# Performance work log

Measured on AMD Instinct MI355X. Metric: run time of the kernel, lower is better.

Reference implementation:

```python
import jax, jax.numpy as jnp
import numpy as np

N_EMBD = 1024
HIDDEN = 4 * N_EMBD          # 4096
ADAPT = HIDDEN // 16         # 256
NUM_EXPERTS = 8
B, S = 4, 2048
LN_EPS = 1e-5


def setup_inputs() -> dict:
    key = jax.random.key(0)
    ks = jax.random.split(key, 8)
    x = jax.random.normal(ks[0], (B, S, N_EMBD), dtype=jnp.float32)
    # top-1 routing: one-hot expert weights (disjoint masks, standard MoE dispatch)
    route = jax.random.randint(ks[1], (B, S), 0, NUM_EXPERTS)
    expert_weights = jax.nn.one_hot(route, NUM_EXPERTS, dtype=jnp.float32)
    up_scale = 0.1 / N_EMBD ** 0.5
    adapt_scale0 = 0.1 / HIDDEN ** 0.5
    adapt_scale = 0.01 / ADAPT ** 0.5
    W_up = jax.random.normal(ks[2], (HIDDEN, N_EMBD), dtype=jnp.float32) * up_scale
    W_adapt = jax.random.normal(ks[3], (ADAPT, HIDDEN), dtype=jnp.float32) * adapt_scale0
    W_exp_adapters = jax.random.normal(ks[4], (NUM_EXPERTS, ADAPT, ADAPT), dtype=jnp.float32) * adapt_scale
    ln_gamma = jnp.ones((NUM_EXPERTS, ADAPT), dtype=jnp.float32)
    ln_beta = jnp.zeros((NUM_EXPERTS, ADAPT), dtype=jnp.float32)
    W_expert_proj = jax.random.normal(ks[5], (HIDDEN, ADAPT), dtype=jnp.float32) * adapt_scale
    W_out = jax.random.normal(ks[6], (N_EMBD, HIDDEN), dtype=jnp.float32) * adapt_scale
    return {"x": x, "expert_weights": expert_weights, "W_up": W_up,
            "W_adapt": W_adapt, "W_exp_adapters": W_exp_adapters,
            "ln_gamma": ln_gamma, "ln_beta": ln_beta,
            "W_expert_proj": W_expert_proj, "W_out": W_out}


def reference(x, expert_weights, W_up, W_adapt, W_exp_adapters, ln_gamma, ln_beta, W_expert_proj, W_out):
    b, s, d = x.shape
    T = b * s
    E = expert_weights.shape[-1]
    xt = x.reshape(T, d)

    # shared MLP path (silu(up_proj(x))) -> output_proj
    h = jax.nn.silu(xt @ W_up.T)                      # [T, HIDDEN]
    shared_out = (h @ W_out.T).reshape(b, s, d)       # [B, S, D]

    active = expert_weights.reshape(T, E) > 0         # [T, E]
    any_active = jnp.any(active, axis=-1)             # [T]
    last_idx = E - 1 - jnp.argmax(active[:, ::-1], axis=-1)  # [T]

    # pre_adapt (silu(up) recomputed == h) -> adapt_proj
    a = h @ W_adapt.T                                 # [T, ADAPT]
    # per-expert adapter linears, then select the winning expert per token
    a_all = jnp.einsum('td,eod->teo', a, W_exp_adapters)      # [T, E, ADAPT]
    a_sel = jnp.take_along_axis(a_all, last_idx[:, None, None], axis=1)[:, 0]  # [T, ADAPT]

    # per-expert LayerNorm params gathered per token
    g = ln_gamma[last_idx]                            # [T, ADAPT]
    be = ln_beta[last_idx]
    mu = jnp.mean(a_sel, axis=-1, keepdims=True)
    var = jnp.mean(jnp.square(a_sel - mu), axis=-1, keepdims=True)
    a_norm = (a_sel - mu) * jax.lax.rsqrt(var + LN_EPS) * g + be

    h2 = a_norm @ W_expert_proj.T                     # [T, HIDDEN]
    e_out = h2 @ W_out.T                              # [T, D]
    combined = jnp.where(any_active[:, None], e_out, 0.0).reshape(b, s, d)
    return shared_out + 0.1 * combined
```

## Files before the change

### kernel.cpp

```cpp
#include <hip/hip_runtime.h>
#include <cstdint>

#define TOK  8192
#define DEMB 1024
#define HID  4096
#define ADP  256
#define NEXP 8
#define KAUG 4352

typedef __bf16 bf16x8 __attribute__((ext_vector_type(8)));
typedef float  f32x4  __attribute__((ext_vector_type(4)));

__device__ __forceinline__ unsigned short f2bf(float f) {
  unsigned int u = __float_as_uint(f);
  u += 0x7fffu + ((u >> 16) & 1u);
  return (unsigned short)(u >> 16);
}
__device__ __forceinline__ float bf2f(unsigned short b) {
  return __uint_as_float(((unsigned int)b) << 16);
}

__global__ __launch_bounds__(256) void convert_all(
    const float* __restrict__ x, const float* __restrict__ wup,
    const float* __restrict__ wout, const float* __restrict__ wadapt,
    const float* __restrict__ wexp, const float* __restrict__ ew,
    const float* __restrict__ wp,
    unsigned short* __restrict__ xb, unsigned short* __restrict__ wub,
    unsigned short* __restrict__ wob, unsigned short* __restrict__ wab,
    unsigned short* __restrict__ web, int* __restrict__ route,
    unsigned short* __restrict__ wpT) {
  __shared__ float tile[64][65];
  int b = blockIdx.x;
  if (b >= 8992) {
    int wli = b - 8992;
    const int h0 = (wli & 63) * 64;
    const int a0 = (wli >> 6) * 64;
    const int t = threadIdx.x;
    const int r = t >> 4;
    const int c = (t & 15) * 4;
#pragma unroll
    for (int p = 0; p < 4; ++p) {
      int row = p * 16 + r;
      float4 v = *(const float4*)(wp + (size_t)(h0 + row) * ADP + a0 + c);
      tile[c + 0][row] = v.x;
      tile[c + 1][row] = v.y;
      tile[c + 2][row] = v.z;
      tile[c + 3][row] = v.w;
    }
    __syncthreads();
#pragma unroll
    for (int q = 0; q < 2; ++q) {
      int idx = q * 256 + t;
      int al = idx >> 3;
      int hg = (idx & 7) * 8;
      unsigned int w0 = (unsigned int)f2bf(tile[al][hg + 0]) |
                        ((unsigned int)f2bf(tile[al][hg + 1]) << 16);
      unsigned int w1 = (unsigned int)f2bf(tile[al][hg + 2]) |
                        ((unsigned int)f2bf(tile[al][hg + 3]) << 16);
      unsigned int w2 = (unsigned int)f2bf(tile[al][hg + 4]) |
                        ((unsigned int)f2bf(tile[al][hg + 5]) << 16);
      unsigned int w3 = (unsigned int)f2bf(tile[al][hg + 6]) |
                        ((unsigned int)f2bf(tile[al][hg + 7]) << 16);
      *(uint4*)(wpT + (size_t)(a0 + al) * HID + h0 + hg) =
          make_uint4(w0, w1, w2, w3);
    }
    return;
  }
  if (b >= 8960) {
    int t = (b - 8960) * 256 + threadIdx.x;
    const float* p = ew + (size_t)t * NEXP;
    int r = -1;
#pragma unroll
    for (int e = 0; e < NEXP; ++e)
      if (p[e] > 0.f) r = e;
    route[t] = r;
    return;
  }
  const float* src; unsigned short* dst; int lb; bool strided = false;
  if      (b < 4096) { src = x;      dst = xb;  lb = b; }
  else if (b < 6144) { src = wup;    dst = wub; lb = b - 4096; }
  else if (b < 8192) { src = wout;   dst = wob; lb = b - 6144; strided = true; }
  else if (b < 8704) { src = wadapt; dst = wab; lb = b - 8192; }
  else               { src = wexp;   dst = web; lb = b - 8704; }
  size_t base = (size_t)lb * 2048;
#pragma unroll
  for (int h = 0; h < 2; ++h) {
    size_t off = base + (size_t)h * 1024 + (size_t)threadIdx.x * 4;
    float4 v = *(const float4*)(src + off);
    ushort4 o;
    o.x = f2bf(v.x); o.y = f2bf(v.y); o.z = f2bf(v.z); o.w = f2bf(v.w);
    size_t doff = strided ? (off >> 12) * KAUG + (off & 4095) : off;
    *(ushort4*)(dst + doff) = o;
  }
}

__device__ __forceinline__ void stage_tile(const unsigned short* __restrict__ g,
                                           int ldg, unsigned short* lds,
                                           int wave, int lane) {
  int srow = lane >> 3;
  int scol = ((lane & 7) ^ (srow & 7)) * 8;
#pragma unroll
  for (int c = 0; c < 4; ++c) {
    int chunk = wave * 4 + c;
    const unsigned short* gp = g + (size_t)(chunk * 8 + srow) * ldg + scol;
    unsigned short* lp = lds + chunk * 512;
    __builtin_amdgcn_global_load_lds(
        (const __attribute__((address_space(1))) unsigned int*)(uintptr_t)gp,
        (__attribute__((address_space(3))) unsigned int*)(uintptr_t)lp,
        16, 0, 0);
  }
}

__device__ __forceinline__ void remap_xcd(int li, int gx, int gy,
                                          int& bx, int& by) {
  int xcd = li & 7;
  int slot = li >> 3;
  bx = slot % gx;
  by = xcd * (gy >> 3) + slot / gx;
}

template <int EPI>
__device__ __forceinline__ void gemm_body(
    int bxr, int byr, int bz,
    const unsigned short* __restrict__ A, int lda,
    const unsigned short* __restrict__ B, int ldb,
    void* __restrict__ C, int ldc,
    const int* __restrict__ route, int kLen, long splitStride,
    unsigned short* As, unsigned short* Bs) {
  const int lane = threadIdx.x & 63;
  const int wave = threadIdx.x >> 6;
  const int wm = wave >> 1, wn = wave & 1;
  const long rowBase = (long)byr * 128;
  const long colBase = (long)bxr * 128;
  const int ks = bz * kLen;
  const unsigned short* Ap = A + rowBase * lda + ks;
  const unsigned short* Bp = B + colBase * ldb + ks;
  f32x4 acc[4][4] = {};

  for (int kt = 0; kt < kLen; kt += 64) {
    stage_tile(Ap + kt, lda, As, wave, lane);
    stage_tile(Bp + kt, ldb, Bs, wave, lane);
    __syncthreads();
#pragma unroll
    for (int kk = 0; kk < 64; kk += 32) {
      const int kb = (kk >> 3) + (lane >> 4);
      const int sw = kb ^ (lane & 7);
      bf16x8 af[4], bfr[4];
#pragma unroll
      for (int mt = 0; mt < 4; ++mt) {
        int m = wm * 64 + mt * 16 + (lane & 15);
        af[mt] = *(const bf16x8*)&As[m * 64 + sw * 8];
      }
#pragma unroll
      for (int nt = 0; nt < 4; ++nt) {
        int n = wn * 64 + nt * 16 + (lane & 15);
        bfr[nt] = *(const bf16x8*)&Bs[n * 64 + sw * 8];
      }
#pragma unroll
      for (int mt = 0; mt < 4; ++mt)
#pragma unroll
        for (int nt = 0; nt < 4; ++nt)
          acc[mt][nt] = __builtin_amdgcn_mfma_f32_16x16x32_bf16(
              af[mt], bfr[nt], acc[mt][nt], 0, 0, 0);
    }
    __syncthreads();
  }

  const int rsub = (lane >> 4) * 4;
  const int csub = lane & 15;
#pragma unroll
  for (int mt = 0; mt < 4; ++mt) {
#pragma unroll
    for (int nt = 0; nt < 4; ++nt) {
      long col = colBase + wn * 64 + nt * 16 + csub;
#pragma unroll
      for (int r = 0; r < 4; ++r) {
        long row = rowBase + wm * 64 + mt * 16 + rsub + r;
        float v = acc[mt][nt][r];
        if (EPI == 0) {
          float s = __fdividef(v, 1.0f + __expf(-v));
          ((unsigned short*)C)[row * ldc + col] = f2bf(s);
        } else if (EPI == 1) {
          ((float*)C + splitStride * bz)[row * ldc + col] = v;
        } else {
          if (route[row] == (int)(col >> 8))
            ((float*)C)[row * ADP + (col & 255)] = v;
        }
      }
    }
  }
}

template <int EPI>
__global__ __launch_bounds__(256, 3) void gemm128(
    const unsigned short* __restrict__ A, int lda,
    const unsigned short* __restrict__ B, int ldb,
    void* __restrict__ C, int ldc,
    const int* __restrict__ route, int kLen, long splitStride) {
  __shared__ unsigned short As[128 * 64];
  __shared__ unsigned short Bs[128 * 64];
  int li = blockIdx.x + gridDim.x * blockIdx.y;
  int bx, by;
  remap_xcd(li, gridDim.x, gridDim.y, bx, by);
  gemm_body<EPI>(bx, by, blockIdx.z, A, lda, B, ldb, C, ldc, route, kLen,
                 splitStride, As, Bs);
}

__global__ __launch_bounds__(256, 3) void gemm_dual(
    const unsigned short* __restrict__ A0, int lda0,
    const unsigned short* __restrict__ B0, int ldb0,
    float* __restrict__ C0, int ldc0, int kLen0, long ss0, int gx0, int gy0,
    int nb0,
    const unsigned short* __restrict__ A1, int lda1,
    const unsigned short* __restrict__ B1, int ldb1,
    float* __restrict__ C1, int ldc1, int kLen1, long ss1, int gx1, int gy1) {
  __shared__ unsigned short As[128 * 64];
  __shared__ unsigned short Bs[128 * 64];
  int li = blockIdx.x;
  if (li < nb0) {
    int per = gx0 * gy0;
    int z = li / per, rem = li % per;
    int bx, by;
    remap_xcd(rem, gx0, gy0, bx, by);
    gemm_body<1>(bx, by, z, A0, lda0, B0, ldb0, C0, ldc0, nullptr, kLen0, ss0,
                 As, Bs);
  } else {
    int wli = li - nb0;
    int per = gx1 * gy1;
    int z = wli / per, rem = wli % per;
    int bx, by;
    remap_xcd(rem, gx1, gy1, bx, by);
    gemm_body<1>(bx, by, z, A1, lda1, B1, ldb1, C1, ldc1, nullptr, kLen1, ss1,
                 As, Bs);
  }
}

__global__ __launch_bounds__(256) void reduce_both(
    const float* __restrict__ P, unsigned short* __restrict__ ab,
    const float* __restrict__ Pw, unsigned short* __restrict__ wob) {
  int b = blockIdx.x;
  if (b < 2048) {
    size_t i = ((size_t)b * 256 + threadIdx.x) * 4;
    const size_t stride = (size_t)TOK * ADP;
    float4 p0 = *(const float4*)(P + i);
    float4 p1 = *(const float4*)(P + stride + i);
    float4 p2 = *(const float4*)(P + 2 * stride + i);
    float4 p3 = *(const float4*)(P + 3 * stride + i);
    ushort4 o;
    o.x = f2bf(p0.x + p1.x + p2.x + p3.x);
    o.y = f2bf(p0.y + p1.y + p2.y + p3.y);
    o.z = f2bf(p0.z + p1.z + p2.z + p3.z);
    o.w = f2bf(p0.w + p1.w + p2.w + p3.w);
    *(ushort4*)(ab + i) = o;
  } else {
    size_t i = ((size_t)(b - 2048) * 256 + threadIdx.x) * 4;
    const size_t stride = (size_t)DEMB * ADP;
    float4 s = *(const float4*)(Pw + i);
#pragma unroll
    for (int k = 1; k < 8; ++k) {
      float4 p = *(const float4*)(Pw + k * stride + i);
      s.x += p.x; s.y += p.y; s.z += p.z; s.w += p.w;
    }
    size_t d = i >> 8, a = i & 255;
    ushort4 o;
    o.x = f2bf(0.1f * s.x); o.y = f2bf(0.1f * s.y);
    o.z = f2bf(0.1f * s.z); o.w = f2bf(0.1f * s.w);
    *(ushort4*)(wob + d * KAUG + HID + a) = o;
  }
}

__global__ __launch_bounds__(256) void ln_kernel(
    const float* __restrict__ asel, const int* __restrict__ route,
    const float* __restrict__ gamma, const float* __restrict__ beta,
    unsigned short* __restrict__ haug) {
  const int lane = threadIdx.x & 63;
  const int t = blockIdx.x * 4 + (threadIdx.x >> 6);
  const int e = route[t];
  float4 v = *(const float4*)(asel + (size_t)t * ADP + lane * 4);
  float s1 = v.x + v.y + v.z + v.w;
  float s2 = v.x * v.x + v.y * v.y + v.z * v.z + v.w * v.w;
#pragma unroll
  for (int off = 32; off > 0; off >>= 1) {
    s1 += __shfl_down(s1, off);
    s2 += __shfl_down(s2, off);
  }
  s1 = __shfl(s1, 0);
  s2 = __shfl(s2, 0);
  float mu = s1 * (1.0f / ADP);
  float var = s2 * (1.0f / ADP) - mu * mu;
  float rstd = rsqrtf(var + 1e-5f);
  ushort4 o;
  if (e >= 0) {
    float4 g = *(const float4*)(gamma + (size_t)e * ADP + lane * 4);
    float4 b = *(const float4*)(beta + (size_t)e * ADP + lane * 4);
    o.x = f2bf((v.x - mu) * rstd * g.x + b.x);
    o.y = f2bf((v.y - mu) * rstd * g.y + b.y);
    o.z = f2bf((v.z - mu) * rstd * g.z + b.z);
    o.w = f2bf((v.w - mu) * rstd * g.w + b.w);
  } else {
    o.x = o.y = o.z = o.w = 0;
  }
  *(ushort4*)(haug + (size_t)t * KAUG + HID + lane * 4) = o;
}

extern "C" void kernel_launch(void* const* d_in, const int* in_sizes, int n_in,
                              void* d_out, int out_size, void* d_ws, size_t ws_size,
                              hipStream_t stream) {
  const float* x     = (const float*)d_in[0];
  const float* ew    = (const float*)d_in[1];
  const float* W_up  = (const float*)d_in[2];
  const float* W_ad  = (const float*)d_in[3];
  const float* W_ex  = (const float*)d_in[4];
  const float* gam   = (const float*)d_in[5];
  const float* bet   = (const float*)d_in[6];
  const float* W_pr  = (const float*)d_in[7];
  const float* W_out = (const float*)d_in[8];
  float* out = (float*)d_out;

  char* ws = (char*)d_ws;
  size_t off = 0;
  auto alloc = [&](size_t n) {
    char* p = ws + off;
    off += (n + 255) & ~(size_t)255;
    return p;
  };
  unsigned short* xb   = (unsigned short*)alloc((size_t)TOK * DEMB * 2);
  unsigned short* wub  = (unsigned short*)alloc((size_t)HID * DEMB * 2);
  unsigned short* wob  = (unsigned short*)alloc((size_t)DEMB * KAUG * 2);
  unsigned short* wab  = (unsigned short*)alloc((size_t)ADP * HID * 2);
  unsigned short* web  = (unsigned short*)alloc((size_t)NEXP * ADP * ADP * 2);
  unsigned short* wpT  = (unsigned short*)alloc((size_t)ADP * HID * 2);
  unsigned short* Haug = (unsigned short*)alloc((size_t)TOK * KAUG * 2);
  float*          P    = (float*)alloc((size_t)4 * TOK * ADP * 4);
  float*          Pw   = (float*)alloc((size_t)8 * DEMB * ADP * 4);
  unsigned short* ab   = (unsigned short*)alloc((size_t)TOK * ADP * 2);
  int*          route  = (int*)alloc((size_t)TOK * 4);
  float* asel = P;

  convert_all<<<9248, 256, 0, stream>>>(x, W_up, W_out, W_ad, W_ex, ew, W_pr,
                                        xb, wub, wob, wab, web, route, wpT);
  gemm128<0><<<dim3(HID / 128, TOK / 128, 1), 256, 0, stream>>>(
      xb, DEMB, wub, DEMB, Haug, KAUG, nullptr, DEMB, 0);
  gemm_dual<<<640, 256, 0, stream>>>(
      Haug, KAUG, wab, HID, P, ADP, HID / 4, (long)TOK * ADP, 2, 64, 512,
      wob, KAUG, wpT, HID, Pw, ADP, HID / 8, (long)DEMB * ADP, 2, 8);
  reduce_both<<<2304, 256, 0, stream>>>(P, ab, Pw, wob);
  gemm128<3><<<dim3(NEXP * ADP / 128, TOK / 128, 1), 256, 0, stream>>>(
      ab, ADP, web, ADP, asel, ADP, route, ADP, 0);
  ln_kernel<<<TOK / 4, 256, 0, stream>>>(asel, route, gam, bet, Haug);
  gemm128<1><<<dim3(DEMB / 128, TOK / 128, 1), 256, 0, stream>>>(
      Haug, KAUG, wob, KAUG, out, DEMB, nullptr, KAUG, 0);
}
```

Before: 346.4 us.

## Add double-buffered 8-wave 128x256 GEMM kernel with phased MFMA scheduling

Adds a new 512-thread GEMM kernel with a 128x256 tile, two LDS buffers and an explicit prefetch schedule. Global-to-LDS loads for the next k-tile are overlapped with MFMA phases, coordinated through barriers, setprio and vmcnt waits. It replaces the single-buffered 128x128 gemm128 for the up-projection, the expert-adapter GEMM and the output GEMM. The aim is to hide memory latency and raise MFMA utilisation. In exchange it uses more LDS per block, lowers occupancy, and depends on a fragile hand-tuned waitcnt schedule.

```diff
diff --git a/kernel.cpp b/kernel.cpp
--- a/kernel.cpp
+++ b/kernel.cpp
@@ -94,6 +94,161 @@
   }
 }
 
+__device__ __forceinline__ void remap_xcd(int li, int gx, int gy,
+                                          int& bx, int& by) {
+  int xcd = li & 7;
+  int slot = li >> 3;
+  bx = slot % gx;
+  by = xcd * (gy >> 3) + slot / gx;
+}
+
+__device__ __forceinline__ void read_frag4(const unsigned short* base, int lane,
+                                           int rowoff, int kk, bf16x8* dst) {
+#pragma unroll
+  for (int i = 0; i < 4; ++i) {
+    int rr = rowoff + i * 16 + (lane & 15);
+    int sw = ((kk >> 3) + (lane >> 4)) ^ (lane & 7);
+    dst[i] = *(const bf16x8*)&base[rr * 64 + sw * 8];
+  }
+}
+
+template <int NH>
+__device__ __forceinline__ void mfma8(const bf16x8* af, const bf16x8* bf,
+                                      f32x4 acc[4][4]) {
+#pragma unroll
+  for (int mt = 0; mt < 4; ++mt)
+#pragma unroll
+    for (int q = 0; q < 2; ++q)
+      acc[mt][NH * 2 + q] = __builtin_amdgcn_mfma_f32_16x16x32_bf16(
+          af[mt], bf[NH * 2 + q], acc[mt][NH * 2 + q], 0, 0, 0);
+}
+
+#define PHASE_MID()                                       \
+  __builtin_amdgcn_s_barrier();                           \
+  asm volatile("s_waitcnt lgkmcnt(0)" ::: "memory");      \
+  __builtin_amdgcn_sched_barrier(0);                      \
+  __builtin_amdgcn_s_setprio(1)
+
+#define PHASE_END()                                       \
+  __builtin_amdgcn_s_setprio(0);                          \
+  __builtin_amdgcn_sched_barrier(0);                      \
+  __builtin_amdgcn_s_barrier()
+
+#define PHASE_END_VM(N)                                   \
+  __builtin_amdgcn_s_setprio(0);                          \
+  __builtin_amdgcn_sched_barrier(0);                      \
+  asm volatile("s_waitcnt vmcnt(" #N ")" ::: "memory");   \
+  __builtin_amdgcn_s_barrier()
+
+template <int EPI>
+__global__ __launch_bounds__(512, 2) void gemm8p(
+    const unsigned short* __restrict__ A, int lda,
+    const unsigned short* __restrict__ B, int ldb,
+    void* __restrict__ C, int ldc, const int* __restrict__ route, int kLen) {
+  __shared__ unsigned short As[2][128 * 64];
+  __shared__ unsigned short Bs[2][256 * 64];
+  const int lane = threadIdx.x & 63;
+  const int wave = threadIdx.x >> 6;
+  const int wm = wave >> 2, wn = wave & 3;
+  int li = blockIdx.x + gridDim.x * blockIdx.y;
+  int bx, by;
+  remap_xcd(li, gridDim.x, gridDim.y, bx, by);
+  const long rowBase = (long)by * 128;
+  const long colBase = (long)bx * 256;
+  const int srow = lane >> 3;
+  const int scol = ((lane & 7) ^ (srow & 7)) * 8;
+  const unsigned short* Ag = A + (rowBase + srow) * (long)lda + scol;
+  const unsigned short* Bg = B + (colBase + srow) * (long)ldb + scol;
+  const int NT = kLen >> 6;
+
+  auto stA = [&](int buf, int t) {
+#pragma unroll
+    for (int c = 0; c < 2; ++c) {
+      int chunk = wave * 2 + c;
+      __builtin_amdgcn_global_load_lds(
+          (const __attribute__((address_space(1))) unsigned int*)(uintptr_t)(
+              Ag + (size_t)chunk * 8 * lda + (size_t)t * 64),
+          (__attribute__((address_space(3))) unsigned int*)(uintptr_t)(
+              &As[buf][chunk * 512]),
+          16, 0, 0);
+    }
+  };
+  auto stB = [&](int buf, int t, int h) {
+#pragma unroll
+    for (int c = 0; c < 2; ++c) {
+      int chunk = h * 16 + wave * 2 + c;
+      __builtin_amdgcn_global_load_lds(
+          (const __attribute__((address_space(1))) unsigned int*)(uintptr_t)(
+              Bg + (size_t)chunk * 8 * ldb + (size_t)t * 64),
+          (__attribute__((address_space(3))) unsigned int*)(uintptr_t)(
+              &Bs[buf][chunk * 512]),
+          16, 0, 0);
+    }
+  };
+
+  f32x4 acc[4][4] = {};
+  bf16x8 af0[4], af1[4], bf0[4], bf1[4];
+
+  stB(0, 0, 0);
+  stB(0, 0, 1);
+  stA(0, 0);
+  if (NT > 1) {
+    stA(1, 1);
+    stB(1, 1, 0);
+    asm volatile("s_waitcnt vmcnt(4)" ::: "memory");
+  } else {
+    asm volatile("s_waitcnt vmcnt(0)" ::: "memory");
+  }
+  __builtin_amdgcn_s_barrier();
+  read_frag4(&As[0][0], lane, wm * 64, 0, af0);
+
+  for (int t = 0; t < NT; ++t) {
+    const int b = t & 1;
+    read_frag4(&Bs[b][0], lane, wn * 64, 0, bf0);
+    if (t + 1 < NT) stB(b ^ 1, t + 1, 1);
+    PHASE_MID();
+    mfma8<0>(af0, bf0, acc);
+    PHASE_END();
+    read_frag4(&As[b][0], lane, wm * 64, 32, af1);
+    PHASE_MID();
+    mfma8<1>(af0, bf0, acc);
+    PHASE_END();
+    read_frag4(&Bs[b][0], lane, wn * 64, 32, bf1);
+    PHASE_MID();
+    mfma8<0>(af1, bf1, acc);
+    PHASE_END_VM(4);
+    if (t + 1 < NT) read_frag4(&As[b ^ 1][0], lane, wm * 64, 0, af0);
+    if (t + 2 < NT) { stA(b, t + 2); stB(b, t + 2, 0); }
+    PHASE_MID();
+    mfma8<1>(af1, bf1, acc);
+    PHASE_END_VM(4);
+  }
+
+  const int rsub = (lane >> 4) * 4;
+  const int csub = lane & 15;
+#pragma unroll
+  for (int mt = 0; mt < 4; ++mt) {
+#pragma unroll
+    for (int nt = 0; nt < 4; ++nt) {
+      long col = colBase + wn * 64 + nt * 16 + csub;
+#pragma unroll
+      for (int r = 0; r < 4; ++r) {
+        long row = rowBase + wm * 64 + mt * 16 + rsub + r;
+        float v = acc[mt][nt][r];
+        if (EPI == 0) {
+          float s = __fdividef(v, 1.0f + __expf(-v));
+          ((unsigned short*)C)[row * ldc + col] = f2bf(s);
+        } else if (EPI == 1) {
+          ((float*)C)[row * ldc + col] = v;
+        } else {
+          if (route[row] == (int)(col >> 8))
+            ((float*)C)[row * ADP + (col & 255)] = v;
+        }
+      }
+    }
+  }
+}
+
 __device__ __forceinline__ void stage_tile(const unsigned short* __restrict__ g,
                                            int ldg, unsigned short* lds,
                                            int wave, int lane) {
@@ -111,21 +266,11 @@
   }
 }
 
-__device__ __forceinline__ void remap_xcd(int li, int gx, int gy,
-                                          int& bx, int& by) {
-  int xcd = li & 7;
-  int slot = li >> 3;
-  bx = slot % gx;
-  by = xcd * (gy >> 3) + slot / gx;
-}
-
-template <int EPI>
-__device__ __forceinline__ void gemm_body(
+__device__ __forceinline__ void gemm_body1(
     int bxr, int byr, int bz,
     const unsigned short* __restrict__ A, int lda,
     const unsigned short* __restrict__ B, int ldb,
-    void* __restrict__ C, int ldc,
-    const int* __restrict__ route, int kLen, long splitStride,
+    float* __restrict__ C, int ldc, int kLen, long splitStride,
     unsigned short* As, unsigned short* Bs) {
   const int lane = threadIdx.x & 63;
   const int wave = threadIdx.x >> 6;
@@ -176,34 +321,10 @@
 #pragma unroll
       for (int r = 0; r < 4; ++r) {
         long row = rowBase + wm * 64 + mt * 16 + rsub + r;
-        float v = acc[mt][nt][r];
-        if (EPI == 0) {
-          float s = __fdividef(v, 1.0f + __expf(-v));
-          ((unsigned short*)C)[row * ldc + col] = f2bf(s);
-        } else if (EPI == 1) {
-          ((float*)C + splitStride * bz)[row * ldc + col] = v;
-        } else {
-          if (route[row] == (int)(col >> 8))
-            ((float*)C)[row * ADP + (col & 255)] = v;
-        }
+        (C + splitStride * bz)[row * ldc + col] = acc[mt][nt][r];
       }
     }
   }
-}
-
-template <int EPI>
-__global__ __launch_bounds__(256, 3) void gemm128(
-    const unsigned short* __restrict__ A, int lda,
-    const unsigned short* __restrict__ B, int ldb,
-    void* __restrict__ C, int ldc,
-    const int* __restrict__ route, int kLen, long splitStride) {
-  __shared__ unsigned short As[128 * 64];
-  __shared__ unsigned short Bs[128 * 64];
-  int li = blockIdx.x + gridDim.x * blockIdx.y;
-  int bx, by;
-  remap_xcd(li, gridDim.x, gridDim.y, bx, by);
-  gemm_body<EPI>(bx, by, blockIdx.z, A, lda, B, ldb, C, ldc, route, kLen,
-                 splitStride, As, Bs);
 }
 
 __global__ __launch_bounds__(256, 3) void gemm_dual(
@@ -222,16 +343,14 @@
     int z = li / per, rem = li % per;
     int bx, by;
     remap_xcd(rem, gx0, gy0, bx, by);
-    gemm_body<1>(bx, by, z, A0, lda0, B0, ldb0, C0, ldc0, nullptr, kLen0, ss0,
-                 As, Bs);
+    gemm_body1(bx, by, z, A0, lda0, B0, ldb0, C0, ldc0, kLen0, ss0, As, Bs);
   } else {
     int wli = li - nb0;
     int per = gx1 * gy1;
     int z = wli / per, rem = wli % per;
     int bx, by;
     remap_xcd(rem, gx1, gy1, bx, by);
-    gemm_body<1>(bx, by, z, A1, lda1, B1, ldb1, C1, ldc1, nullptr, kLen1, ss1,
-                 As, Bs);
+    gemm_body1(bx, by, z, A1, lda1, B1, ldb1, C1, ldc1, kLen1, ss1, As, Bs);
   }
 }
 
@@ -339,15 +458,15 @@
 
   convert_all<<<9248, 256, 0, stream>>>(x, W_up, W_out, W_ad, W_ex, ew, W_pr,
                                         xb, wub, wob, wab, web, route, wpT);
-  gemm128<0><<<dim3(HID / 128, TOK / 128, 1), 256, 0, stream>>>(
-      xb, DEMB, wub, DEMB, Haug, KAUG, nullptr, DEMB, 0);
+  gemm8p<0><<<dim3(HID / 256, TOK / 128, 1), 512, 0, stream>>>(
+      xb, DEMB, wub, DEMB, Haug, KAUG, nullptr, DEMB);
   gemm_dual<<<640, 256, 0, stream>>>(
       Haug, KAUG, wab, HID, P, ADP, HID / 4, (long)TOK * ADP, 2, 64, 512,
       wob, KAUG, wpT, HID, Pw, ADP, HID / 8, (long)DEMB * ADP, 2, 8);
   reduce_both<<<2304, 256, 0, stream>>>(P, ab, Pw, wob);
-  gemm128<3><<<dim3(NEXP * ADP / 128, TOK / 128, 1), 256, 0, stream>>>(
-      ab, ADP, web, ADP, asel, ADP, route, ADP, 0);
+  gemm8p<3><<<dim3(NEXP * ADP / 256, TOK / 128, 1), 512, 0, stream>>>(
+      ab, ADP, web, ADP, asel, ADP, route, ADP);
   ln_kernel<<<TOK / 4, 256, 0, stream>>>(asel, route, gam, bet, Haug);
-  gemm128<1><<<dim3(DEMB / 128, TOK / 128, 1), 256, 0, stream>>>(
-      Haug, KAUG, wob, KAUG, out, DEMB, nullptr, KAUG, 0);
-}
+  gemm8p<1><<<dim3(DEMB / 256, TOK / 128, 1), 512, 0, stream>>>(
+      Haug, KAUG, wob, KAUG, out, DEMB, nullptr, KAUG);
+}
```

After: 359.3 us. +3.7%, slower.
